# Optimization experiments

Hardware: AMD Instinct MI355X
Metric: run time of the kernel (lower is better)

The kernel has to match this reference:

```python
import jax, jax.numpy as jnp
import numpy as np
from jax import lax

DIM = 128
DEPTH = 2
OUT_DIM = 256
DIM_HEAD = 64
HEADS = 8
WS = 16
INNER = DIM_HEAD * HEADS
EPS = 1e-5
SCALE = DIM_HEAD ** (-0.5)


def setup_inputs() -> dict:
    key = jax.random.key(0)
    ks = jax.random.split(key, 20)
    s = 0.02
    L = DEPTH
    inp = {
        "x": jax.random.normal(ks[0], (1, DIM, 256, 256), dtype=jnp.float32),
        "ln1_g": jnp.ones((L, DIM), dtype=jnp.float32),
        "ln1_b": jnp.zeros((L, DIM), dtype=jnp.float32),
        "wq": jax.random.normal(ks[1], (L, INNER, DIM), dtype=jnp.float32) * s,
        "wkv": jax.random.normal(ks[2], (L, 2 * INNER, DIM), dtype=jnp.float32) * s,
        "wo": jax.random.normal(ks[3], (L, DIM, INNER), dtype=jnp.float32) * s,
        "bo": jnp.zeros((L, DIM), dtype=jnp.float32),
        "ln2_g": jnp.ones((L, DIM), dtype=jnp.float32),
        "ln2_b": jnp.zeros((L, DIM), dtype=jnp.float32),
        "w_in": jax.random.normal(ks[4], (L, DIM, DIM), dtype=jnp.float32) * s,
        "b_in": jnp.zeros((L, DIM), dtype=jnp.float32),
        "w_c3": jax.random.normal(ks[5], (L, OUT_DIM, DIM, 3, 3), dtype=jnp.float32) * s,
        "b_c3": jnp.zeros((L, OUT_DIM), dtype=jnp.float32),
        "w_c1": jax.random.normal(ks[6], (L, DIM, OUT_DIM), dtype=jnp.float32) * s,
        "b_c1": jnp.zeros((L, DIM), dtype=jnp.float32),
        "w_outer": jax.random.normal(ks[7], (DIM, DIM), dtype=jnp.float32) * s,
        "b_outer": jnp.zeros((DIM,), dtype=jnp.float32),
    }
    return inp


def _layernorm(x, g, b):
    # channel-wise (dim=1) norm; note torch code uses (std + eps), not sqrt(var + eps)
    mean = jnp.mean(x, axis=1, keepdims=True)
    std = jnp.sqrt(jnp.var(x, axis=1, keepdims=True))
    return (x - mean) / (std + EPS) * g[None, :, None, None] + b[None, :, None, None]


def _conv1x1(w, x, b=None):
    y = jnp.einsum('oi,bihw->bohw', w, x)
    if b is not None:
        y = y + b[None, :, None, None]
    return y


def _to_windows(t, B, H, W):
    # [B, HEADS*DIM_HEAD, H, W] -> [B*HEADS*nx*ny, WS*WS, DIM_HEAD]
    nx, ny = H // WS, W // WS
    t = t.reshape(B, HEADS, DIM_HEAD, nx, WS, ny, WS)
    t = t.transpose(0, 1, 3, 5, 4, 6, 2)
    return t.reshape(B * HEADS * nx * ny, WS * WS, DIM_HEAD)


def _from_windows(t, B, H, W):
    nx, ny = H // WS, W // WS
    t = t.reshape(B, HEADS, nx, ny, WS, WS, DIM_HEAD)
    t = t.transpose(0, 1, 6, 2, 4, 3, 5)
    return t.reshape(B, HEADS * DIM_HEAD, H, W)


def _attention(x, wq_l, wkv_l, wo_l, bo_l):
    B, _, H, W = x.shape
    q = _conv1x1(wq_l, x)
    kv = _conv1x1(wkv_l, x)
    k, v = kv[:, :INNER], kv[:, INNER:]
    q = _to_windows(q, B, H, W)
    k = _to_windows(k, B, H, W)
    v = _to_windows(v, B, H, W)
    sim = jnp.einsum('bid,bjd->bij', q, k) * SCALE  # [nwin, 256, 256]
    attn = jax.nn.softmax(sim, axis=-1)
    out = jnp.einsum('bij,bjd->bid', attn, v)
    out = _from_windows(out, B, H, W)
    return _conv1x1(wo_l, out, bo_l)


def _feedforward(x, w_in_l, b_in_l, w_c3_l, b_c3_l, w_c1_l, b_c1_l):
    h = _conv1x1(w_in_l, x, b_in_l)
    h = lax.conv_general_dilated(h, w_c3_l, window_strides=(1, 1), padding='SAME',
                                 dimension_numbers=('NCHW', 'OIHW', 'NCHW'))
    h = h + b_c3_l[None, :, None, None]
    h = jax.nn.gelu(h, approximate=False)
    return _conv1x1(w_c1_l, h, b_c1_l)


def reference(x, ln1_g, ln1_b, wq, wkv, wo, bo, ln2_g, ln2_b,
              w_in, b_in, w_c3, b_c3, w_c1, b_c1, w_outer, b_outer):
    for l in range(DEPTH):
        xn = _layernorm(x, ln1_g[l], ln1_b[l])
        x = _attention(xn, wq[l], wkv[l], wo[l], bo[l]) + x
        xn = _layernorm(x, ln2_g[l], ln2_b[l])
        x = _feedforward(xn, w_in[l], b_in[l], w_c3[l], b_c3[l], w_c1[l], b_c1[l]) + x
    return _conv1x1(w_outer, x, b_outer) + x
```

## Files before the change

### kernel.cpp

```cpp
#include <hip/hip_runtime.h>
#include <hip/hip_bf16.h>
#include <math.h>

typedef __hip_bfloat16 bf16;
typedef float f4 __attribute__((ext_vector_type(4)));
typedef short s8 __attribute__((ext_vector_type(8)));
typedef unsigned int u2 __attribute__((ext_vector_type(2)));
typedef unsigned int u4v __attribute__((ext_vector_type(4)));

__device__ __forceinline__ void gload16(const void* g, char* l) {
  __builtin_amdgcn_global_load_lds(
      (const __attribute__((address_space(1))) unsigned int*)g,
      (__attribute__((address_space(3))) unsigned int*)l, 16, 0, 0);
}
__device__ __forceinline__ unsigned short bfr(float f) {
  bf16 h = __float2bfloat16(f);
  return *(unsigned short*)&h;
}
__device__ __forceinline__ unsigned int pk2(float a, float b) {
  return (unsigned int)bfr(a) | ((unsigned int)bfr(b) << 16);
}
__device__ __forceinline__ unsigned int pkt(float a, float b) {
  return __builtin_amdgcn_perm(__float_as_uint(b), __float_as_uint(a), 0x07060302u);
}

__global__ __launch_bounds__(256) void prep_w(
    const float* __restrict__ wq, const float* __restrict__ wkv,
    const float* __restrict__ wo, const float* __restrict__ win,
    const float* __restrict__ wc3, const float* __restrict__ wc1,
    const float* __restrict__ wout, ushort* __restrict__ cw)
{
  int i = blockIdx.x * 256 + threadIdx.x;
  float v;
  if (i < 131072) v = wq[i];
  else if (i < 393216) v = wkv[i - 131072];
  else if (i < 524288) v = wo[i - 393216];
  else if (i < 557056) v = win[i - 524288];
  else if (i < 1146880) {
    int j = i - 557056; int lyr = j / 294912; int r = j - lyr * 294912;
    int m = r / 1152; int k = r - m * 1152; int tap = k >> 7; int ic = k & 127;
    v = wc3[(((size_t)lyr * 256 + m) * 128 + ic) * 9 + tap];
  }
  else if (i < 1212416) v = wc1[i - 1146880];
  else if (i < 1228800) v = wout[i - 1212416];
  else if (i < 1230848) { cw[i] = 0; return; }
  else return;
  cw[i] = bfr(v);
}

template<bool NCHW>
__global__ __launch_bounds__(256) void ln_nhwc(
    const float* __restrict__ x, const float* __restrict__ g,
    const float* __restrict__ b, ushort* __restrict__ y)
{
  const int p = blockIdx.x * 256 + threadIdx.x;
  f4 v[32];
  float s = 0.f, s2 = 0.f;
  if constexpr (NCHW) {
#pragma unroll
    for (int i = 0; i < 32; ++i)
#pragma unroll
      for (int j = 0; j < 4; ++j) {
        float t = x[(size_t)(i * 4 + j) * 65536 + p];
        v[i][j] = t; s += t; s2 += t * t;
      }
  } else {
    const f4* base = (const f4*)(x + (size_t)p * 128);
#pragma unroll
    for (int i = 0; i < 32; ++i) {
      v[i] = base[i];
#pragma unroll
      for (int j = 0; j < 4; ++j) { s += v[i][j]; s2 += v[i][j] * v[i][j]; }
    }
  }
  float mean = s * (1.f / 128.f);
  float var = s2 * (1.f / 128.f) - mean * mean;
  var = var > 0.f ? var : 0.f;
  float inv = 1.f / (sqrtf(var) + 1e-5f);
  u2* dst = (u2*)(y + (size_t)p * 128);
#pragma unroll
  for (int i = 0; i < 32; ++i) {
    f4 gg = *(const f4*)(g + i * 4);
    f4 bb = *(const f4*)(b + i * 4);
    float f0 = (v[i][0] - mean) * inv * gg[0] + bb[0];
    float f1 = (v[i][1] - mean) * inv * gg[1] + bb[1];
    float f2 = (v[i][2] - mean) * inv * gg[2] + bb[2];
    float f3 = (v[i][3] - mean) * inv * gg[3] + bb[3];
    u2 st; st.x = pk2(f0, f1); st.y = pk2(f2, f3);
    dst[i] = st;
  }
}

template<int MODE>
__global__ __launch_bounds__(256) void gemm_nhwc(
    const ushort* __restrict__ A, const ushort* __restrict__ X,
    const float* __restrict__ bias, const float* __restrict__ res,
    void* __restrict__ out, ushort* __restrict__ out2, const int K, const int M)
{
  __shared__ __align__(16) char sm[32768];
  const int tid = threadIdx.x, w = tid >> 6, l = tid & 63;
  const int quad = l >> 4, l15 = l & 15;
  const int n0 = blockIdx.x * 128, m0 = blockIdx.y * 128;
  const int mh = (w & 1) * 64, nh = (w >> 1) * 64;
  const f4 fz = {0.f, 0.f, 0.f, 0.f};
  f4 acc[4][4];
#pragma unroll
  for (int a = 0; a < 4; ++a)
#pragma unroll
    for (int b2 = 0; b2 < 4; ++b2) acc[a][b2] = fz;

  const int KI = K >> 6;
  for (int kk = 0; kk < KI; ++kk) {
    if (kk) __syncthreads();
    const int k0 = kk << 6;
#pragma unroll
    for (int j = 0; j < 4; ++j) {
      int p = j * 256 + tid, r = p >> 3, c = (p & 7) ^ (r & 7);
      gload16(A + (size_t)(m0 + r) * K + k0 + c * 8, sm + (j * 256 + w * 64) * 16);
    }
#pragma unroll
    for (int j = 0; j < 4; ++j) {
      int p = j * 256 + tid, r = p >> 3, c = (p & 7) ^ (r & 7);
      gload16(X + (size_t)(n0 + r) * K + k0 + c * 8, sm + 16384 + (j * 256 + w * 64) * 16);
    }
    __syncthreads();
#pragma unroll
    for (int ks = 0; ks < 2; ++ks) {
      s8 af[4], bx[4];
#pragma unroll
      for (int mt = 0; mt < 4; ++mt) {
        int rr = mh + mt * 16 + l15;
        af[mt] = *(const s8*)(sm + rr * 128 + (((ks * 4 + quad) ^ (rr & 7)) << 4));
      }
#pragma unroll
      for (int nt = 0; nt < 4; ++nt) {
        int rr = nh + nt * 16 + l15;
        bx[nt] = *(const s8*)(sm + 16384 + rr * 128 + (((ks * 4 + quad) ^ (rr & 7)) << 4));
      }
#pragma unroll
      for (int mt = 0; mt < 4; ++mt)
#pragma unroll
        for (int nt = 0; nt < 4; ++nt)
          acc[mt][nt] = __builtin_amdgcn_mfma_f32_16x16x32_bf16(af[mt], bx[nt], acc[mt][nt], 0, 0, 0);
    }
  }
#pragma unroll
  for (int mt = 0; mt < 4; ++mt) {
#pragma unroll
    for (int nt = 0; nt < 4; ++nt) {
      const int m = m0 + mh + mt * 16 + quad * 4;
      const int n = n0 + nh + nt * 16 + l15;
      f4 bb = *(const f4*)(bias + m);
      f4 v = acc[mt][nt] + bb;
      if constexpr (MODE == 0) {
        u2 st; st.x = pk2(v[0], v[1]); st.y = pk2(v[2], v[3]);
        *(u2*)((ushort*)out + (size_t)n * M + m) = st;
      } else if constexpr (MODE == 1 || MODE == 3) {
        f4 r = *(const f4*)(res + (size_t)n * M + m);
        v += r;
        *(f4*)((float*)out + (size_t)n * M + m) = v;
        if constexpr (MODE == 3) {
          u2 st; st.x = pk2(v[0], v[1]); st.y = pk2(v[2], v[3]);
          *(u2*)(out2 + (size_t)n * M + m) = st;
        }
      } else if constexpr (MODE == 4) {
        f4 r;
#pragma unroll
        for (int i = 0; i < 4; ++i) r[i] = res[(size_t)(m + i) * 65536 + n];
        v += r;
        *(f4*)((float*)out + (size_t)n * M + m) = v;
      } else {
        f4 r = *(const f4*)(res + (size_t)n * M + m);
#pragma unroll
        for (int i = 0; i < 4; ++i)
          ((float*)out)[(size_t)(m + i) * 65536 + n] = v[i] + r[i];
      }
    }
  }
}

__global__ __launch_bounds__(256) void conv3_kernel(
    const ushort* __restrict__ A, const ushort* __restrict__ X,
    const float* __restrict__ bias, ushort* __restrict__ out,
    const ushort* __restrict__ zp)
{
  __shared__ __align__(16) char sm[32768];
  const int tid = threadIdx.x, w = tid >> 6, l = tid & 63;
  const int quad = l >> 4, l15 = l & 15;
  const int n0 = blockIdx.x * 128, m0 = blockIdx.y * 128;
  const int mh = (w & 1) * 64, nh = (w >> 1) * 64;
  const f4 fz = {0.f, 0.f, 0.f, 0.f};
  f4 acc[4][4];
#pragma unroll
  for (int a = 0; a < 4; ++a)
#pragma unroll
    for (int b2 = 0; b2 < 4; ++b2) acc[a][b2] = fz;

  for (int kk = 0; kk < 18; ++kk) {
    if (kk) __syncthreads();
    const int tap = kk >> 1, ky = tap / 3, kx = tap - ky * 3;
    const int dn = (ky - 1) * 256 + (kx - 1);
    const int kseg = (kk & 1) << 6;
#pragma unroll
    for (int j = 0; j < 4; ++j) {
      int p = j * 256 + tid, r = p >> 3, c = (p & 7) ^ (r & 7);
      gload16(A + (size_t)(m0 + r) * 1152 + kk * 64 + c * 8, sm + (j * 256 + w * 64) * 16);
    }
#pragma unroll
    for (int j = 0; j < 4; ++j) {
      int p = j * 256 + tid, r = p >> 3, c = (p & 7) ^ (r & 7);
      int nl = n0 + r;
      int ys = (nl >> 8) + ky - 1, xs = (nl & 255) + kx - 1;
      const ushort* gp = ((unsigned)ys < 256u && (unsigned)xs < 256u)
                         ? X + (size_t)(nl + dn) * 128 + kseg + c * 8 : zp;
      gload16(gp, sm + 16384 + (j * 256 + w * 64) * 16);
    }
    __syncthreads();
#pragma unroll
    for (int ks = 0; ks < 2; ++ks) {
      s8 af[4], bx[4];
#pragma unroll
      for (int mt = 0; mt < 4; ++mt) {
        int rr = mh + mt * 16 + l15;
        af[mt] = *(const s8*)(sm + rr * 128 + (((ks * 4 + quad) ^ (rr & 7)) << 4));
      }
#pragma unroll
      for (int nt = 0; nt < 4; ++nt) {
        int rr = nh + nt * 16 + l15;
        bx[nt] = *(const s8*)(sm + 16384 + rr * 128 + (((ks * 4 + quad) ^ (rr & 7)) << 4));
      }
#pragma unroll
      for (int mt = 0; mt < 4; ++mt)
#pragma unroll
        for (int nt = 0; nt < 4; ++nt)
          acc[mt][nt] = __builtin_amdgcn_mfma_f32_16x16x32_bf16(af[mt], bx[nt], acc[mt][nt], 0, 0, 0);
    }
  }
#pragma unroll
  for (int mt = 0; mt < 4; ++mt) {
#pragma unroll
    for (int nt = 0; nt < 4; ++nt) {
      const int m = m0 + mh + mt * 16 + quad * 4;
      const int n = n0 + nh + nt * 16 + l15;
      f4 bb = *(const f4*)(bias + m);
      f4 v = acc[mt][nt] + bb;
      float g0 = 0.5f * v[0] * (1.f + erff(v[0] * 0.70710678118f));
      float g1 = 0.5f * v[1] * (1.f + erff(v[1] * 0.70710678118f));
      float g2 = 0.5f * v[2] * (1.f + erff(v[2] * 0.70710678118f));
      float g3 = 0.5f * v[3] * (1.f + erff(v[3] * 0.70710678118f));
      u2 st; st.x = pk2(g0, g1); st.y = pk2(g2, g3);
      *(u2*)(out + (size_t)n * 256 + m) = st;
    }
  }
}

__global__ __launch_bounds__(256, 2) void attn_kernel(
    const ushort* __restrict__ xn, const ushort* __restrict__ wq,
    const ushort* __restrict__ wkv, ushort* __restrict__ ao)
{
  __shared__ __align__(16) char sm[65536];
  char* RK  = sm;
  char* RVT = sm + 32768;
  const int tid = threadIdx.x, w = tid >> 6, l = tid & 63;
  const int quad = l >> 4, l15 = l & 15;
  const int win = blockIdx.x, head = blockIdx.y;
  const int nbase = ((win >> 4) << 12) + ((win & 15) << 4);
  const f4 fz = {0.f, 0.f, 0.f, 0.f};

  s8 bx[4][4];
#pragma unroll
  for (int nt = 0; nt < 4; ++nt) {
    int tok = w * 64 + nt * 16 + l15;
    const char* rowp = (const char*)(xn + (size_t)(nbase + ((tok >> 4) << 8) + (tok & 15)) * 128);
#pragma unroll
    for (int ks = 0; ks < 4; ++ks)
      bx[nt][ks] = *(const s8*)(rowp + (ks * 4 + quad) * 16);
  }
  const char* wqp = (const char*)(wq + (size_t)head * 64 * 128);
  const char* wkp = (const char*)(wkv + (size_t)head * 64 * 128);
  const char* wvp = (const char*)(wkv + (size_t)(512 + head * 64) * 128);

  s8 bq[4][2];
  {
    f4 acc[4][4];
#pragma unroll
    for (int a = 0; a < 4; ++a)
#pragma unroll
      for (int b2 = 0; b2 < 4; ++b2) acc[a][b2] = fz;
#pragma unroll
    for (int ks = 0; ks < 4; ++ks) {
      s8 aw[4];
#pragma unroll
      for (int mt = 0; mt < 4; ++mt)
        aw[mt] = *(const s8*)(wqp + (size_t)(mt * 16 + l15) * 256 + (ks * 4 + quad) * 16);
#pragma unroll
      for (int mt = 0; mt < 4; ++mt)
#pragma unroll
        for (int nt = 0; nt < 4; ++nt)
          acc[mt][nt] = __builtin_amdgcn_mfma_f32_16x16x32_bf16(aw[mt], bx[nt][ks], acc[mt][nt], 0, 0, 0);
    }
#pragma unroll
    for (int nt = 0; nt < 4; ++nt) {
      unsigned pd[4][2];
#pragma unroll
      for (int mt = 0; mt < 4; ++mt) {
        pd[mt][0] = pkt(acc[mt][nt][0], acc[mt][nt][1]);
        pd[mt][1] = pkt(acc[mt][nt][2], acc[mt][nt][3]);
      }
#pragma unroll
      for (int ks2 = 0; ks2 < 2; ++ks2) {
        u4v t;
#pragma unroll
        for (int dj = 0; dj < 4; ++dj) {
          int srcl = l15 + (((quad & 1) * 2 + (dj >> 1)) << 4);
          unsigned va = (unsigned)__shfl((int)pd[2 * ks2][dj & 1], srcl, 64);
          unsigned vb = (unsigned)__shfl((int)pd[2 * ks2 + 1][dj & 1], srcl, 64);
          t[dj] = (quad < 2) ? va : vb;
        }
        bq[nt][ks2] = __builtin_bit_cast(s8, t);
      }
    }
  }

  {
    f4 acc[4][4];
#pragma unroll
    for (int a = 0; a < 4; ++a)
#pragma unroll
      for (int b2 = 0; b2 < 4; ++b2) acc[a][b2] = fz;
#pragma unroll
    for (int ks = 0; ks < 4; ++ks) {
      s8 aw[4];
#pragma unroll
      for (int mt = 0; mt < 4; ++mt)
        aw[mt] = *(const s8*)(wkp + (size_t)(mt * 16 + l15) * 256 + (ks * 4 + quad) * 16);
#pragma unroll
      for (int mt = 0; mt < 4; ++mt)
#pragma unroll
        for (int nt = 0; nt < 4; ++nt)
          acc[mt][nt] = __builtin_amdgcn_mfma_f32_16x16x32_bf16(aw[mt], bx[nt][ks], acc[mt][nt], 0, 0, 0);
    }
#pragma unroll
    for (int mt = 0; mt < 4; ++mt)
#pragma unroll
      for (int nt = 0; nt < 4; ++nt) {
        int tok = w * 64 + nt * 16 + l15, d0 = mt * 16 + quad * 4;
        char* a = RK + tok * 128 + (((d0 >> 3) ^ (tok & 7)) << 4) + (d0 & 7) * 2;
        *(unsigned int*)a = pkt(acc[mt][nt][0], acc[mt][nt][1]);
        *(unsigned int*)(a + 4) = pkt(acc[mt][nt][2], acc[mt][nt][3]);
      }
  }

  {
    f4 acc[4][4];
#pragma unroll
    for (int a = 0; a < 4; ++a)
#pragma unroll
      for (int b2 = 0; b2 < 4; ++b2) acc[a][b2] = fz;
#pragma unroll
    for (int ks = 0; ks < 4; ++ks) {
      s8 bw[4];
#pragma unroll
      for (int nt = 0; nt < 4; ++nt)
        bw[nt] = *(const s8*)(wvp + (size_t)(nt * 16 + l15) * 256 + (ks * 4 + quad) * 16);
#pragma unroll
      for (int mt = 0; mt < 4; ++mt)
#pragma unroll
        for (int nt = 0; nt < 4; ++nt)
          acc[mt][nt] = __builtin_amdgcn_mfma_f32_16x16x32_bf16(bx[mt][ks], bw[nt], acc[mt][nt], 0, 0, 0);
    }
#pragma unroll
    for (int mt = 0; mt < 4; ++mt)
#pragma unroll
      for (int nt = 0; nt < 4; ++nt) {
        int d = nt * 16 + l15, t0 = w * 64 + mt * 16 + quad * 4;
        char* a = RVT + d * 512 + (((t0 >> 3) ^ (d & 31)) << 4) + (t0 & 7) * 2;
        *(unsigned int*)a = pkt(acc[mt][nt][0], acc[mt][nt][1]);
        *(unsigned int*)(a + 4) = pkt(acc[mt][nt][2], acc[mt][nt][3]);
      }
  }
  __syncthreads();

  f4 o[4][4];
  float lsum[4] = {0.f, 0.f, 0.f, 0.f};
#pragma unroll
  for (int a = 0; a < 4; ++a)
#pragma unroll
    for (int b2 = 0; b2 < 4; ++b2) o[a][b2] = fz;

  for (int jt = 0; jt < 4; ++jt) {
    f4 s[4][4];
#pragma unroll
    for (int a = 0; a < 4; ++a)
#pragma unroll
      for (int b2 = 0; b2 < 4; ++b2) s[a][b2] = fz;
#pragma unroll
    for (int ks2 = 0; ks2 < 2; ++ks2) {
      s8 af[4];
#pragma unroll
      for (int mt = 0; mt < 4; ++mt) {
        int rr = jt * 64 + mt * 16 + l15;
        af[mt] = *(const s8*)(RK + rr * 128 + (((ks2 * 4 + quad) ^ (rr & 7)) << 4));
      }
#pragma unroll
      for (int mt = 0; mt < 4; ++mt)
#pragma unroll
        for (int nt = 0; nt < 4; ++nt)
          s[mt][nt] = __builtin_amdgcn_mfma_f32_16x16x32_bf16(af[mt], bq[nt][ks2], s[mt][nt], 0, 0, 0);
    }
    s8 Pt[4][2];
#pragma unroll
    for (int nt = 0; nt < 4; ++nt) {
      unsigned pd[4][2];
#pragma unroll
      for (int mt = 0; mt < 4; ++mt) {
        float e0 = exp2f(s[mt][nt][0] * 0.18033688f);
        float e1 = exp2f(s[mt][nt][1] * 0.18033688f);
        float e2 = exp2f(s[mt][nt][2] * 0.18033688f);
        float e3 = exp2f(s[mt][nt][3] * 0.18033688f);
        lsum[nt] += e0 + e1 + e2 + e3;
        pd[mt][0] = pkt(e0, e1);
        pd[mt][1] = pkt(e2, e3);
      }
#pragma unroll
      for (int ks2 = 0; ks2 < 2; ++ks2) {
        u4v t;
#pragma unroll
        for (int dj = 0; dj < 4; ++dj) {
          int srcl = l15 + (((quad & 1) * 2 + (dj >> 1)) << 4);
          unsigned va = (unsigned)__shfl((int)pd[2 * ks2][dj & 1], srcl, 64);
          unsigned vb = (unsigned)__shfl((int)pd[2 * ks2 + 1][dj & 1], srcl, 64);
          t[dj] = (quad < 2) ? va : vb;
        }
        Pt[nt][ks2] = __builtin_bit_cast(s8, t);
      }
    }
#pragma unroll
    for (int ks2 = 0; ks2 < 2; ++ks2) {
      s8 av[4];
#pragma unroll
      for (int mt = 0; mt < 4; ++mt) {
        int d = mt * 16 + l15;
        av[mt] = *(const s8*)(RVT + d * 512 + (((jt * 8 + ks2 * 4 + quad) ^ (d & 31)) << 4));
      }
#pragma unroll
      for (int mt = 0; mt < 4; ++mt)
#pragma unroll
        for (int nt = 0; nt < 4; ++nt)
          o[mt][nt] = __builtin_amdgcn_mfma_f32_16x16x32_bf16(av[mt], Pt[nt][ks2], o[mt][nt], 0, 0, 0);
    }
  }

  float inv[4];
#pragma unroll
  for (int nt = 0; nt < 4; ++nt) {
    float v = lsum[nt];
    v += __shfl_xor(v, 16, 64);
    v += __shfl_xor(v, 32, 64);
    inv[nt] = 1.f / v;
  }
#pragma unroll
  for (int nt = 0; nt < 4; ++nt) {
    int i = w * 64 + nt * 16 + l15;
    int n = nbase + ((i >> 4) << 8) + (i & 15);
    ushort* dst = ao + (size_t)n * 512 + head * 64 + quad * 4;
#pragma unroll
    for (int mt = 0; mt < 4; ++mt) {
      u2 st;
      st.x = pkt(o[mt][nt][0] * inv[nt], o[mt][nt][1] * inv[nt]);
      st.y = pkt(o[mt][nt][2] * inv[nt], o[mt][nt][3] * inv[nt]);
      *(u2*)(dst + mt * 16) = st;
    }
  }
}

extern "C" void kernel_launch(void* const* d_in, const int* in_sizes, int n_in,
                              void* d_out, int out_size, void* d_ws, size_t ws_size,
                              hipStream_t stream)
{
  const float* x_in    = (const float*)d_in[0];
  const float* ln1_g   = (const float*)d_in[1];
  const float* ln1_b   = (const float*)d_in[2];
  const float* wq      = (const float*)d_in[3];
  const float* wkv     = (const float*)d_in[4];
  const float* wo      = (const float*)d_in[5];
  const float* bo      = (const float*)d_in[6];
  const float* ln2_g   = (const float*)d_in[7];
  const float* ln2_b   = (const float*)d_in[8];
  const float* w_in    = (const float*)d_in[9];
  const float* b_in    = (const float*)d_in[10];
  const float* w_c3    = (const float*)d_in[11];
  const float* b_c3    = (const float*)d_in[12];
  const float* w_c1    = (const float*)d_in[13];
  const float* b_c1    = (const float*)d_in[14];
  const float* w_outer = (const float*)d_in[15];
  const float* b_outer = (const float*)d_in[16];

  char* wsb = (char*)d_ws;
  ushort* CW = (ushort*)wsb;
  float*  XH = (float*)(wsb + 4194304);
  ushort* XN = (ushort*)(wsb + 37748736);
  ushort* AO = (ushort*)(wsb + 54525952);
  ushort* H  = (ushort*)(wsb + 121634816);
  ushort* G  = (ushort*)(wsb + 138412032);
  ushort* XB = (ushort*)(wsb + 171966464);

  const ushort* zp = CW + 1228800;
  dim3 b256(256);

  prep_w<<<dim3(4808), b256, 0, stream>>>(wq, wkv, wo, w_in, w_c3, w_c1, w_outer, CW);

  for (int lyr = 0; lyr < 2; ++lyr) {
    const ushort* cwq = CW + lyr * 65536;
    const ushort* cwkv = CW + 131072 + lyr * 131072;
    const ushort* cwo = CW + 393216 + lyr * 65536;
    const ushort* cwin = CW + 524288 + lyr * 16384;
    const ushort* cw3 = CW + 557056 + lyr * 294912;
    const ushort* cwc1 = CW + 1146880 + lyr * 32768;

    if (lyr == 0)
      ln_nhwc<true><<<dim3(256), b256, 0, stream>>>(x_in, ln1_g, ln1_b, XN);
    else
      ln_nhwc<false><<<dim3(256), b256, 0, stream>>>(XH, ln1_g + lyr * 128, ln1_b + lyr * 128, XN);

    attn_kernel<<<dim3(256, 8), dim3(256), 0, stream>>>(XN, cwq, cwkv, AO);

    if (lyr == 0)
      gemm_nhwc<4><<<dim3(512, 1), b256, 0, stream>>>(cwo, AO, bo, x_in, XH, nullptr, 512, 128);
    else
      gemm_nhwc<1><<<dim3(512, 1), b256, 0, stream>>>(cwo, AO, bo + lyr * 128, XH, XH, nullptr, 512, 128);

    ln_nhwc<false><<<dim3(256), b256, 0, stream>>>(XH, ln2_g + lyr * 128, ln2_b + lyr * 128, XN);
    gemm_nhwc<0><<<dim3(512, 1), b256, 0, stream>>>(cwin, XN, b_in + lyr * 128, nullptr, H, nullptr, 128, 128);
    conv3_kernel<<<dim3(512, 2), b256, 0, stream>>>(cw3, H, b_c3 + lyr * 256, G, zp);

    if (lyr == 1)
      gemm_nhwc<3><<<dim3(512, 1), b256, 0, stream>>>(cwc1, G, b_c1 + lyr * 128, XH, XH, XB, 256, 128);
    else
      gemm_nhwc<1><<<dim3(512, 1), b256, 0, stream>>>(cwc1, G, b_c1 + lyr * 128, XH, XH, nullptr, 256, 128);
  }
  gemm_nhwc<2><<<dim3(512, 1), b256, 0, stream>>>(CW + 1212416, XB, b_outer, XH, d_out, nullptr, 128, 128);
}
```

Measured before the change: 674.2 us.

## Fuse layernorm into residual GEMM epilogues and stage softmax probabilities through LDS

The residual-add GEMM epilogues now compute the per-pixel channel layernorm with a cross-wave LDS reduction and write the normalized bf16 activations directly. This removes three standalone layernorm passes over the fp32 residual stream. The attention kernel also replaces the cross-lane shuffle transpose of the probability tile with per-wave LDS staging in half-tile chunks. That adds 16KB of shared memory, which may lower occupancy, and an extra block barrier in the GEMM epilogue.

```diff
diff --git a/kernel.cpp b/kernel.cpp
--- a/kernel.cpp
+++ b/kernel.cpp
@@ -48,31 +48,20 @@
   cw[i] = bfr(v);
 }
 
-template<bool NCHW>
-__global__ __launch_bounds__(256) void ln_nhwc(
+__global__ __launch_bounds__(256) void ln_nchw(
     const float* __restrict__ x, const float* __restrict__ g,
     const float* __restrict__ b, ushort* __restrict__ y)
 {
   const int p = blockIdx.x * 256 + threadIdx.x;
   f4 v[32];
   float s = 0.f, s2 = 0.f;
-  if constexpr (NCHW) {
-#pragma unroll
-    for (int i = 0; i < 32; ++i)
-#pragma unroll
-      for (int j = 0; j < 4; ++j) {
-        float t = x[(size_t)(i * 4 + j) * 65536 + p];
-        v[i][j] = t; s += t; s2 += t * t;
-      }
-  } else {
-    const f4* base = (const f4*)(x + (size_t)p * 128);
-#pragma unroll
-    for (int i = 0; i < 32; ++i) {
-      v[i] = base[i];
-#pragma unroll
-      for (int j = 0; j < 4; ++j) { s += v[i][j]; s2 += v[i][j] * v[i][j]; }
-    }
-  }
+#pragma unroll
+  for (int i = 0; i < 32; ++i)
+#pragma unroll
+    for (int j = 0; j < 4; ++j) {
+      float t = x[(size_t)(i * 4 + j) * 65536 + p];
+      v[i][j] = t; s += t; s2 += t * t;
+    }
   float mean = s * (1.f / 128.f);
   float var = s2 * (1.f / 128.f) - mean * mean;
   var = var > 0.f ? var : 0.f;
@@ -95,9 +84,12 @@
 __global__ __launch_bounds__(256) void gemm_nhwc(
     const ushort* __restrict__ A, const ushort* __restrict__ X,
     const float* __restrict__ bias, const float* __restrict__ res,
-    void* __restrict__ out, ushort* __restrict__ out2, const int K, const int M)
+    void* __restrict__ out, ushort* __restrict__ out2,
+    const float* __restrict__ lg, const float* __restrict__ lb,
+    const int K, const int M)
 {
   __shared__ __align__(16) char sm[32768];
+  __shared__ float red[4][4][16][2];
   const int tid = threadIdx.x, w = tid >> 6, l = tid & 63;
   const int quad = l >> 4, l15 = l & 15;
   const int n0 = blockIdx.x * 128, m0 = blockIdx.y * 128;
@@ -144,36 +136,87 @@
           acc[mt][nt] = __builtin_amdgcn_mfma_f32_16x16x32_bf16(af[mt], bx[nt], acc[mt][nt], 0, 0, 0);
     }
   }
-#pragma unroll
-  for (int mt = 0; mt < 4; ++mt) {
+
+  f4 v[4][4];
+#pragma unroll
+  for (int mt = 0; mt < 4; ++mt)
 #pragma unroll
     for (int nt = 0; nt < 4; ++nt) {
       const int m = m0 + mh + mt * 16 + quad * 4;
       const int n = n0 + nh + nt * 16 + l15;
-      f4 bb = *(const f4*)(bias + m);
-      f4 v = acc[mt][nt] + bb;
+      f4 t = acc[mt][nt] + *(const f4*)(bias + m);
+      if constexpr (MODE == 2 || MODE == 3 || MODE == 5)
+        t += *(const f4*)(res + (size_t)n * M + m);
+      if constexpr (MODE == 6) {
+#pragma unroll
+        for (int i = 0; i < 4; ++i) t[i] += res[(size_t)(m + i) * 65536 + n];
+      }
+      v[mt][nt] = t;
+    }
+
+#pragma unroll
+  for (int mt = 0; mt < 4; ++mt)
+#pragma unroll
+    for (int nt = 0; nt < 4; ++nt) {
+      const int m = m0 + mh + mt * 16 + quad * 4;
+      const int n = n0 + nh + nt * 16 + l15;
       if constexpr (MODE == 0) {
-        u2 st; st.x = pk2(v[0], v[1]); st.y = pk2(v[2], v[3]);
+        u2 st; st.x = pk2(v[mt][nt][0], v[mt][nt][1]); st.y = pk2(v[mt][nt][2], v[mt][nt][3]);
         *(u2*)((ushort*)out + (size_t)n * M + m) = st;
-      } else if constexpr (MODE == 1 || MODE == 3) {
-        f4 r = *(const f4*)(res + (size_t)n * M + m);
-        v += r;
-        *(f4*)((float*)out + (size_t)n * M + m) = v;
+      } else if constexpr (MODE == 2) {
+#pragma unroll
+        for (int i = 0; i < 4; ++i)
+          ((float*)out)[(size_t)(m + i) * 65536 + n] = v[mt][nt][i];
+      } else {
+        *(f4*)((float*)out + (size_t)n * M + m) = v[mt][nt];
         if constexpr (MODE == 3) {
-          u2 st; st.x = pk2(v[0], v[1]); st.y = pk2(v[2], v[3]);
+          u2 st; st.x = pk2(v[mt][nt][0], v[mt][nt][1]); st.y = pk2(v[mt][nt][2], v[mt][nt][3]);
           *(u2*)(out2 + (size_t)n * M + m) = st;
         }
-      } else if constexpr (MODE == 4) {
-        f4 r;
-#pragma unroll
-        for (int i = 0; i < 4; ++i) r[i] = res[(size_t)(m + i) * 65536 + n];
-        v += r;
-        *(f4*)((float*)out + (size_t)n * M + m) = v;
-      } else {
-        f4 r = *(const f4*)(res + (size_t)n * M + m);
-#pragma unroll
-        for (int i = 0; i < 4; ++i)
-          ((float*)out)[(size_t)(m + i) * 65536 + n] = v[i] + r[i];
+      }
+    }
+
+  if constexpr (MODE == 5 || MODE == 6) {
+    float s1[4], s2v[4];
+#pragma unroll
+    for (int nt = 0; nt < 4; ++nt) {
+      float a = 0.f, b2 = 0.f;
+#pragma unroll
+      for (int mt = 0; mt < 4; ++mt)
+#pragma unroll
+        for (int i = 0; i < 4; ++i) { float t = v[mt][nt][i]; a += t; b2 += t * t; }
+      a += __shfl_xor(a, 16, 64);  b2 += __shfl_xor(b2, 16, 64);
+      a += __shfl_xor(a, 32, 64);  b2 += __shfl_xor(b2, 32, 64);
+      s1[nt] = a; s2v[nt] = b2;
+    }
+    if (quad == 0) {
+#pragma unroll
+      for (int nt = 0; nt < 4; ++nt) {
+        red[w][nt][l15][0] = s1[nt];
+        red[w][nt][l15][1] = s2v[nt];
+      }
+    }
+    __syncthreads();
+#pragma unroll
+    for (int nt = 0; nt < 4; ++nt) {
+      float t1 = s1[nt] + red[w ^ 1][nt][l15][0];
+      float t2 = s2v[nt] + red[w ^ 1][nt][l15][1];
+      float mean = t1 * (1.f / 128.f);
+      float var = t2 * (1.f / 128.f) - mean * mean;
+      var = var > 0.f ? var : 0.f;
+      float inv = 1.f / (sqrtf(var) + 1e-5f);
+      const int n = n0 + nh + nt * 16 + l15;
+#pragma unroll
+      for (int mt = 0; mt < 4; ++mt) {
+        const int m = mh + mt * 16 + quad * 4;
+        f4 gg = *(const f4*)(lg + m);
+        f4 bb = *(const f4*)(lb + m);
+        float f0 = (v[mt][nt][0] - mean) * inv * gg[0] + bb[0];
+        float f1 = (v[mt][nt][1] - mean) * inv * gg[1] + bb[1];
+        float f2 = (v[mt][nt][2] - mean) * inv * gg[2] + bb[2];
+        float f3 = (v[mt][nt][3] - mean) * inv * gg[3] + bb[3];
+        u2 st; st.x = pk2(f0, f1); st.y = pk2(f2, f3);
+        *(u2*)(out2 + (size_t)n * 128 + m) = st;
       }
     }
   }
@@ -258,11 +301,12 @@
     const ushort* __restrict__ xn, const ushort* __restrict__ wq,
     const ushort* __restrict__ wkv, ushort* __restrict__ ao)
 {
-  __shared__ __align__(16) char sm[65536];
+  __shared__ __align__(16) char sm[81920];
   char* RK  = sm;
   char* RVT = sm + 32768;
   const int tid = threadIdx.x, w = tid >> 6, l = tid & 63;
   const int quad = l >> 4, l15 = l & 15;
+  char* Pw  = sm + 65536 + w * 4096;
   const int win = blockIdx.x, head = blockIdx.y;
   const int nbase = ((win >> 4) << 12) + ((win & 15) << 4);
   const f4 fz = {0.f, 0.f, 0.f, 0.f};
@@ -389,65 +433,58 @@
     for (int b2 = 0; b2 < 4; ++b2) o[a][b2] = fz;
 
   for (int jt = 0; jt < 4; ++jt) {
-    f4 s[4][4];
-#pragma unroll
-    for (int a = 0; a < 4; ++a)
-#pragma unroll
-      for (int b2 = 0; b2 < 4; ++b2) s[a][b2] = fz;
-#pragma unroll
-    for (int ks2 = 0; ks2 < 2; ++ks2) {
-      s8 af[4];
-#pragma unroll
-      for (int mt = 0; mt < 4; ++mt) {
-        int rr = jt * 64 + mt * 16 + l15;
-        af[mt] = *(const s8*)(RK + rr * 128 + (((ks2 * 4 + quad) ^ (rr & 7)) << 4));
-      }
-#pragma unroll
-      for (int mt = 0; mt < 4; ++mt)
-#pragma unroll
-        for (int nt = 0; nt < 4; ++nt)
-          s[mt][nt] = __builtin_amdgcn_mfma_f32_16x16x32_bf16(af[mt], bq[nt][ks2], s[mt][nt], 0, 0, 0);
-    }
-    s8 Pt[4][2];
-#pragma unroll
-    for (int nt = 0; nt < 4; ++nt) {
-      unsigned pd[4][2];
-#pragma unroll
-      for (int mt = 0; mt < 4; ++mt) {
-        float e0 = exp2f(s[mt][nt][0] * 0.18033688f);
-        float e1 = exp2f(s[mt][nt][1] * 0.18033688f);
-        float e2 = exp2f(s[mt][nt][2] * 0.18033688f);
-        float e3 = exp2f(s[mt][nt][3] * 0.18033688f);
-        lsum[nt] += e0 + e1 + e2 + e3;
-        pd[mt][0] = pkt(e0, e1);
-        pd[mt][1] = pkt(e2, e3);
-      }
-#pragma unroll
-      for (int ks2 = 0; ks2 < 2; ++ks2) {
-        u4v t;
-#pragma unroll
-        for (int dj = 0; dj < 4; ++dj) {
-          int srcl = l15 + (((quad & 1) * 2 + (dj >> 1)) << 4);
-          unsigned va = (unsigned)__shfl((int)pd[2 * ks2][dj & 1], srcl, 64);
-          unsigned vb = (unsigned)__shfl((int)pd[2 * ks2 + 1][dj & 1], srcl, 64);
-          t[dj] = (quad < 2) ? va : vb;
+#pragma unroll
+    for (int half = 0; half < 2; ++half) {
+      f4 s[2][4];
+#pragma unroll
+      for (int a = 0; a < 2; ++a)
+#pragma unroll
+        for (int b2 = 0; b2 < 4; ++b2) s[a][b2] = fz;
+#pragma unroll
+      for (int kd = 0; kd < 2; ++kd) {
+        s8 af[2];
+#pragma unroll
+        for (int m2 = 0; m2 < 2; ++m2) {
+          int rr = jt * 64 + (half * 2 + m2) * 16 + l15;
+          af[m2] = *(const s8*)(RK + rr * 128 + (((kd * 4 + quad) ^ (rr & 7)) << 4));
         }
-        Pt[nt][ks2] = __builtin_bit_cast(s8, t);
-      }
-    }
-#pragma unroll
-    for (int ks2 = 0; ks2 < 2; ++ks2) {
-      s8 av[4];
+#pragma unroll
+        for (int m2 = 0; m2 < 2; ++m2)
+#pragma unroll
+          for (int nt = 0; nt < 4; ++nt)
+            s[m2][nt] = __builtin_amdgcn_mfma_f32_16x16x32_bf16(af[m2], bq[nt][kd], s[m2][nt], 0, 0, 0);
+      }
+#pragma unroll
+      for (int m2 = 0; m2 < 2; ++m2)
+#pragma unroll
+        for (int nt = 0; nt < 4; ++nt) {
+          float e0 = exp2f(s[m2][nt][0] * 0.18033688f);
+          float e1 = exp2f(s[m2][nt][1] * 0.18033688f);
+          float e2 = exp2f(s[m2][nt][2] * 0.18033688f);
+          float e3 = exp2f(s[m2][nt][3] * 0.18033688f);
+          lsum[nt] += e0 + e1 + e2 + e3;
+          int iL = nt * 16 + l15;
+          int jp = m2 * 16 + quad * 4;
+          char* a = Pw + iL * 64 + (((jp >> 3) ^ (iL & 3)) << 4) + (jp & 7) * 2;
+          *(unsigned int*)a = pkt(e0, e1);
+          *(unsigned int*)(a + 4) = pkt(e2, e3);
+        }
+      s8 bp[4], av[4];
+#pragma unroll
+      for (int nt = 0; nt < 4; ++nt) {
+        int iL = nt * 16 + l15;
+        bp[nt] = *(const s8*)(Pw + iL * 64 + ((quad ^ (iL & 3)) << 4));
+      }
 #pragma unroll
       for (int mt = 0; mt < 4; ++mt) {
         int d = mt * 16 + l15;
-        av[mt] = *(const s8*)(RVT + d * 512 + (((jt * 8 + ks2 * 4 + quad) ^ (d & 31)) << 4));
+        av[mt] = *(const s8*)(RVT + d * 512 + (((jt * 8 + half * 4 + quad) ^ (d & 31)) << 4));
       }
 #pragma unroll
       for (int mt = 0; mt < 4; ++mt)
 #pragma unroll
         for (int nt = 0; nt < 4; ++nt)
-          o[mt][nt] = __builtin_amdgcn_mfma_f32_16x16x32_bf16(av[mt], Pt[nt][ks2], o[mt][nt], 0, 0, 0);
+          o[mt][nt] = __builtin_amdgcn_mfma_f32_16x16x32_bf16(av[mt], bp[nt], o[mt][nt], 0, 0, 0);
     }
   }
 
@@ -510,34 +547,25 @@
 
   prep_w<<<dim3(4808), b256, 0, stream>>>(wq, wkv, wo, w_in, w_c3, w_c1, w_outer, CW);
 
-  for (int lyr = 0; lyr < 2; ++lyr) {
-    const ushort* cwq = CW + lyr * 65536;
-    const ushort* cwkv = CW + 131072 + lyr * 131072;
-    const ushort* cwo = CW + 393216 + lyr * 65536;
-    const ushort* cwin = CW + 524288 + lyr * 16384;
-    const ushort* cw3 = CW + 557056 + lyr * 294912;
-    const ushort* cwc1 = CW + 1146880 + lyr * 32768;
-
-    if (lyr == 0)
-      ln_nhwc<true><<<dim3(256), b256, 0, stream>>>(x_in, ln1_g, ln1_b, XN);
-    else
-      ln_nhwc<false><<<dim3(256), b256, 0, stream>>>(XH, ln1_g + lyr * 128, ln1_b + lyr * 128, XN);
-
-    attn_kernel<<<dim3(256, 8), dim3(256), 0, stream>>>(XN, cwq, cwkv, AO);
-
-    if (lyr == 0)
-      gemm_nhwc<4><<<dim3(512, 1), b256, 0, stream>>>(cwo, AO, bo, x_in, XH, nullptr, 512, 128);
-    else
-      gemm_nhwc<1><<<dim3(512, 1), b256, 0, stream>>>(cwo, AO, bo + lyr * 128, XH, XH, nullptr, 512, 128);
-
-    ln_nhwc<false><<<dim3(256), b256, 0, stream>>>(XH, ln2_g + lyr * 128, ln2_b + lyr * 128, XN);
-    gemm_nhwc<0><<<dim3(512, 1), b256, 0, stream>>>(cwin, XN, b_in + lyr * 128, nullptr, H, nullptr, 128, 128);
-    conv3_kernel<<<dim3(512, 2), b256, 0, stream>>>(cw3, H, b_c3 + lyr * 256, G, zp);
-
-    if (lyr == 1)
-      gemm_nhwc<3><<<dim3(512, 1), b256, 0, stream>>>(cwc1, G, b_c1 + lyr * 128, XH, XH, XB, 256, 128);
-    else
-      gemm_nhwc<1><<<dim3(512, 1), b256, 0, stream>>>(cwc1, G, b_c1 + lyr * 128, XH, XH, nullptr, 256, 128);
-  }
-  gemm_nhwc<2><<<dim3(512, 1), b256, 0, stream>>>(CW + 1212416, XB, b_outer, XH, d_out, nullptr, 128, 128);
-}
+  ln_nchw<<<dim3(256), b256, 0, stream>>>(x_in, ln1_g, ln1_b, XN);
+  attn_kernel<<<dim3(256, 8), b256, 0, stream>>>(XN, CW, CW + 131072, AO);
+  gemm_nhwc<6><<<dim3(512, 1), b256, 0, stream>>>(
+      CW + 393216, AO, bo, x_in, XH, XN, ln2_g, ln2_b, 512, 128);
+  gemm_nhwc<0><<<dim3(512, 1), b256, 0, stream>>>(
+      CW + 524288, XN, b_in, nullptr, H, nullptr, nullptr, nullptr, 128, 128);
+  conv3_kernel<<<dim3(512, 2), b256, 0, stream>>>(CW + 557056, H, b_c3, G, zp);
+  gemm_nhwc<5><<<dim3(512, 1), b256, 0, stream>>>(
+      CW + 1146880, G, b_c1, XH, XH, XN, ln1_g + 128, ln1_b + 128, 256, 128);
+
+  attn_kernel<<<dim3(256, 8), b256, 0, stream>>>(XN, CW + 65536, CW + 262144, AO);
+  gemm_nhwc<5><<<dim3(512, 1), b256, 0, stream>>>(
+      CW + 458752, AO, bo + 128, XH, XH, XN, ln2_g + 128, ln2_b + 128, 512, 128);
+  gemm_nhwc<0><<<dim3(512, 1), b256, 0, stream>>>(
+      CW + 540672, XN, b_in + 128, nullptr, H, nullptr, nullptr, nullptr, 128, 128);
+  conv3_kernel<<<dim3(512, 2), b256, 0, stream>>>(CW + 851968, H, b_c3 + 256, G, zp);
+  gemm_nhwc<3><<<dim3(512, 1), b256, 0, stream>>>(
+      CW + 1179648, G, b_c1 + 128, XH, XH, XB, nullptr, nullptr, 256, 128);
+
+  gemm_nhwc<2><<<dim3(512, 1), b256, 0, stream>>>(
+      CW + 1212416, XB, b_outer, XH, d_out, nullptr, nullptr, nullptr, 128, 128);
+}
```

Result: no change. 680.9 us (+1.0%).
